# Kernel optimization log

Hardware: AMD Instinct MI355X
Metric: run time of the kernel (lower is better)

The kernel has to match this reference:

```python
import jax, jax.numpy as jnp
import numpy as np

B, N, D, H, K, R = 128, 2048, 256, 16, 32, 16
LEAKY_SLOPE = 0.01


def setup_inputs() -> dict:
    key = jax.random.key(0)
    ks = jax.random.split(key, 8)
    s = 0.05
    inp = jax.random.normal(ks[0], (B * N, D), dtype=jnp.float32)
    batch_ids = jnp.repeat(jnp.arange(B, dtype=jnp.int32), N)  # equal-size graphs
    Wk = jax.random.normal(ks[1], (K, D), dtype=jnp.float32) * s
    Wq0 = jax.random.normal(ks[2], (H * K, D), dtype=jnp.float32) * s
    Wq1 = jax.random.normal(ks[3], (H * K, D), dtype=jnp.float32) * s
    We = jax.random.normal(ks[4], (R, D), dtype=jnp.float32) * s
    Wout = jax.random.normal(ks[5], (D, H * R), dtype=jnp.float32) * s
    bout = jax.random.normal(ks[6], (D,), dtype=jnp.float32) * s
    return {"inp": inp, "batch_ids": batch_ids, "Wk": Wk, "Wq0": Wq0,
            "Wq1": Wq1, "We": We, "Wout": Wout, "bout": bout}


def reference(inp, batch_ids, Wk, Wq0, Wq1, We, Wout, bout):
    b = int(jnp.max(batch_ids)) + 1  # number of graphs (static at trace time)
    d = inp.shape[-1]
    # global max pool per graph (torch_geometric global_max_pool)
    pooled = jax.ops.segment_max(inp, batch_ids, num_segments=b)  # [B, D]
    x = inp.reshape(b, -1, d)                                     # [B, N, D]
    keys = jnp.einsum('bnd,kd->bnk', x, Wk)                       # [B, N, K]

    def head_embed(Wq):
        q = (pooled @ Wq.T).reshape(b, H, K)                      # [B, H, K]
        logits = jnp.einsum('bhk,bnk->bhn', q, keys)              # [B, H, N]
        att = jax.nn.softmax(logits, axis=-1)
        feat = jnp.einsum('bhn,bnd->bhd', att, x)                 # [B, H, D]
        return jnp.einsum('bhd,rd->bhr', feat, We)                # [B, H, R]

    dx = (head_embed(Wq0) - head_embed(Wq1)).reshape(b, -1)       # [B, H*R]
    out = dx @ Wout.T + bout
    return jnp.where(out >= 0, out, LEAKY_SLOPE * out)            # LeakyReLU
```

## Files before the change

### kernel.cpp

```cpp
#include <hip/hip_runtime.h>
#include <math.h>

#define B_ 128
#define N_ 2048
#define D_ 256
#define NHEADS 32
#define CHUNK 128
#define NCH 16

#define POOLEDP_OFF 0
#define PHI_OFF     524288
#define PLO_OFF     1048576
#define ML_OFF      1572864
#define FEATP_OFF   1703936

#define XHI_S  0
#define XLO_S  65536
#define ATT_S  131072
#define SMAX_S 139776
#define SSUM_S 140800
#define LDS_BYTES 141824

typedef __attribute__((ext_vector_type(8))) short short8;
typedef __attribute__((ext_vector_type(4))) float f32x4;

__device__ __forceinline__ unsigned short f2bf(float f) {
    unsigned u = __float_as_uint(f);
    u += 0x7fff + ((u >> 16) & 1);
    return (unsigned short)(u >> 16);
}
__device__ __forceinline__ float bf2f(unsigned short h) {
    return __uint_as_float(((unsigned)h) << 16);
}
__device__ __forceinline__ unsigned pack2bf(float a, float b) {
    return (unsigned)f2bf(a) | ((unsigned)f2bf(b) << 16);
}
__device__ __forceinline__ unsigned xsw(int row) {
    return (unsigned)((row ^ (row >> 3)) & 7) << 4;
}

__global__ __launch_bounds__(256) void k_pool(const float* __restrict__ inp,
                                              float* __restrict__ pooledp) {
    int b = blockIdx.x >> 4;
    int ch = blockIdx.x & 15;
    int t = threadIdx.x;
    int sub = t >> 6;
    int dq = (t & 63) * 4;
    const float* p = inp + ((size_t)(b * N_ + ch * 128 + sub)) * D_ + dq;
    float4 m = {-INFINITY, -INFINITY, -INFINITY, -INFINITY};
#pragma unroll 4
    for (int i = 0; i < 32; ++i) {
        float4 v = *(const float4*)(p + (size_t)i * 4 * D_);
        m.x = fmaxf(m.x, v.x); m.y = fmaxf(m.y, v.y);
        m.z = fmaxf(m.z, v.z); m.w = fmaxf(m.w, v.w);
    }
    __shared__ float sm[4 * 256];
    sm[sub * 256 + dq + 0] = m.x;
    sm[sub * 256 + dq + 1] = m.y;
    sm[sub * 256 + dq + 2] = m.z;
    sm[sub * 256 + dq + 3] = m.w;
    __syncthreads();
    float v = fmaxf(fmaxf(sm[t], sm[256 + t]), fmaxf(sm[512 + t], sm[768 + t]));
    pooledp[((size_t)ch * B_ + b) * 256 + t] = v;
}

__global__ __launch_bounds__(256) void k_qp(const float* __restrict__ pooledp,
                                            const float* __restrict__ Wq0,
                                            const float* __restrict__ Wq1,
                                            const float* __restrict__ Wk,
                                            unsigned short* __restrict__ Phi,
                                            unsigned short* __restrict__ Plo) {
    __shared__ float pl[D_];
    __shared__ float ql[1024];
    int b = blockIdx.x, t = threadIdx.x;
    float pv = -INFINITY;
#pragma unroll
    for (int i = 0; i < 16; ++i)
        pv = fmaxf(pv, pooledp[((size_t)i * B_ + b) * 256 + t]);
    pl[t] = pv;
    __syncthreads();
    for (int rep = 0; rep < 4; ++rep) {
        int idx = rep * 256 + t;
        const float* Wq = (idx < 512) ? Wq0 : Wq1;
        int row = idx & 511;
        const float4* wr = (const float4*)(Wq + (size_t)row * D_);
        float acc = 0.0f;
        for (int dqi = 0; dqi < 64; ++dqi) {
            float4 w = wr[dqi];
            const float* pp = &pl[dqi * 4];
            acc += w.x * pp[0] + w.y * pp[1] + w.z * pp[2] + w.w * pp[3];
        }
        ql[idx] = acc;
    }
    __syncthreads();
    float wk[32];
#pragma unroll
    for (int k = 0; k < 32; ++k) wk[k] = Wk[k * D_ + t];
    for (int j = 0; j < NHEADS; ++j) {
        const float* q = &ql[(j >> 4) * 512 + (j & 15) * 32];
        float acc = 0.0f;
#pragma unroll
        for (int k = 0; k < 32; ++k) acc = fmaf(q[k], wk[k], acc);
        unsigned short hi = f2bf(acc);
        unsigned short lo = f2bf(acc - bf2f(hi));
        Phi[((size_t)b * NHEADS + j) * D_ + t] = hi;
        Plo[((size_t)b * NHEADS + j) * D_ + t] = lo;
    }
}

__global__ __launch_bounds__(512, 2) void k_attn(const float* __restrict__ inp,
                                                 const unsigned short* __restrict__ Phi,
                                                 const unsigned short* __restrict__ Plo,
                                                 float* __restrict__ ml,
                                                 float* __restrict__ featp) {
    extern __shared__ unsigned char smem[];
    float* smax = (float*)(smem + SMAX_S);
    float* ssum = (float*)(smem + SSUM_S);

    int b = blockIdx.x >> 4, ns = blockIdx.x & 15;
    int t = threadIdx.x;
    int w = t >> 6;
    int lane = t & 63;
    int lq = lane >> 4;
    int lm = lane & 15;
    size_t gnode0 = (size_t)b * N_ + (size_t)ns * CHUNK;

#pragma unroll
    for (int i = 0; i < 16; ++i) {
        int row = i * 8 + w;
        float4 v = *(const float4*)(inp + (gnode0 + row) * D_ + lane * 4);
        ushort4 h4, l4;
        h4.x = f2bf(v.x); l4.x = f2bf(v.x - bf2f(h4.x));
        h4.y = f2bf(v.y); l4.y = f2bf(v.y - bf2f(h4.y));
        h4.z = f2bf(v.z); l4.z = f2bf(v.z - bf2f(h4.z));
        h4.w = f2bf(v.w); l4.w = f2bf(v.w - bf2f(h4.w));
        unsigned byteoff = (unsigned)row * 512u + (((unsigned)lane * 8u) ^ xsw(row));
        *(ushort4*)(smem + XHI_S + byteoff) = h4;
        *(ushort4*)(smem + XLO_S + byteoff) = l4;
    }
    __syncthreads();

    f32x4 acc_s[2];
    acc_s[0] = (f32x4){0.f, 0.f, 0.f, 0.f};
    acc_s[1] = (f32x4){0.f, 0.f, 0.f, 0.f};
    int arow = w * 16 + lm;
    unsigned abase = (unsigned)arow * 512u;
    unsigned asl = xsw(arow);
#pragma unroll
    for (int dc = 0; dc < 8; ++dc) {
        short8 bh[2], bl[2];
#pragma unroll
        for (int ht = 0; ht < 2; ++ht) {
            size_t poff = ((size_t)b * NHEADS + ht * 16 + lm) * D_ + dc * 32 + lq * 8;
            bh[ht] = *(const short8*)(Phi + poff);
            bl[ht] = *(const short8*)(Plo + poff);
        }
        unsigned doff = (((unsigned)(dc * 32 + lq * 8)) * 2u) ^ asl;
        short8 ah = *(const short8*)(smem + XHI_S + abase + doff);
        short8 al = *(const short8*)(smem + XLO_S + abase + doff);
#pragma unroll
        for (int ht = 0; ht < 2; ++ht) {
            acc_s[ht] = __builtin_amdgcn_mfma_f32_16x16x32_bf16(ah, bh[ht], acc_s[ht], 0, 0, 0);
            acc_s[ht] = __builtin_amdgcn_mfma_f32_16x16x32_bf16(ah, bl[ht], acc_s[ht], 0, 0, 0);
            acc_s[ht] = __builtin_amdgcn_mfma_f32_16x16x32_bf16(al, bh[ht], acc_s[ht], 0, 0, 0);
        }
    }

    float bm[2];
#pragma unroll
    for (int ht = 0; ht < 2; ++ht) {
        float m = fmaxf(fmaxf(acc_s[ht][0], acc_s[ht][1]),
                        fmaxf(acc_s[ht][2], acc_s[ht][3]));
        m = fmaxf(m, __shfl_xor(m, 16));
        m = fmaxf(m, __shfl_xor(m, 32));
        if (lane < 16) smax[w * 32 + ht * 16 + lane] = m;
    }
    __syncthreads();
#pragma unroll
    for (int ht = 0; ht < 2; ++ht) {
        float mm = smax[ht * 16 + lm];
#pragma unroll
        for (int w2 = 1; w2 < 8; ++w2) mm = fmaxf(mm, smax[w2 * 32 + ht * 16 + lm]);
        bm[ht] = mm;
    }
#pragma unroll
    for (int ht = 0; ht < 2; ++ht) {
        float e0 = __expf(acc_s[ht][0] - bm[ht]);
        float e1 = __expf(acc_s[ht][1] - bm[ht]);
        float e2 = __expf(acc_s[ht][2] - bm[ht]);
        float e3 = __expf(acc_s[ht][3] - bm[ht]);
        float s = (e0 + e1) + (e2 + e3);
        uint2 pk;
        pk.x = pack2bf(e0, e1);
        pk.y = pack2bf(e2, e3);
        *(uint2*)(smem + ATT_S + (size_t)(ht * 16 + lm) * 272 + w * 32 + lq * 8) = pk;
        s += __shfl_xor(s, 16);
        s += __shfl_xor(s, 32);
        if (lane < 16) ssum[w * 32 + ht * 16 + lane] = s;
    }
    __syncthreads();
    if (t < 32) {
        float mB = smax[t];
        float l = ssum[t];
#pragma unroll
        for (int w2 = 1; w2 < 8; ++w2) {
            mB = fmaxf(mB, smax[w2 * 32 + t]);
            l += ssum[w2 * 32 + t];
        }
        float* mlp = ml + ((size_t)(b * NHEADS + t) * NCH + ns) * 2;
        mlp[0] = mB;
        mlp[1] = l;
    }

    f32x4 acc_o[2][2];
#pragma unroll
    for (int ht = 0; ht < 2; ++ht)
#pragma unroll
        for (int dt = 0; dt < 2; ++dt) acc_o[ht][dt] = (f32x4){0.f, 0.f, 0.f, 0.f};

    int d0w = w * 32;
#pragma unroll
    for (int c = 0; c < 4; ++c) {
        short8 a0 = *(const short8*)(smem + ATT_S + (size_t)lm * 272 + c * 64 + lq * 16);
        short8 a1 = *(const short8*)(smem + ATT_S + (size_t)(16 + lm) * 272 + c * 64 + lq * 16);
#pragma unroll
        for (int dt = 0; dt < 2; ++dt) {
            unsigned d2 = (unsigned)(d0w + dt * 16 + lm) * 2u;
            int n0 = c * 32 + lq * 8;
            short8 bf;
#pragma unroll
            for (int j = 0; j < 8; ++j) {
                int n = n0 + j;
                unsigned byteoff = (unsigned)n * 512u + (d2 ^ xsw(n));
                bf[j] = *(const short*)(smem + XHI_S + byteoff);
            }
            acc_o[0][dt] = __builtin_amdgcn_mfma_f32_16x16x32_bf16(a0, bf, acc_o[0][dt], 0, 0, 0);
            acc_o[1][dt] = __builtin_amdgcn_mfma_f32_16x16x32_bf16(a1, bf, acc_o[1][dt], 0, 0, 0);
        }
    }
    float* fb = featp + ((size_t)(ns * B_ + b)) * D_ * NHEADS;
#pragma unroll
    for (int ht = 0; ht < 2; ++ht)
#pragma unroll
        for (int dt = 0; dt < 2; ++dt) {
            int d = d0w + dt * 16 + lm;
            int h0 = ht * 16 + lq * 4;
            *(f32x4*)(fb + (size_t)d * NHEADS + h0) = acc_o[ht][dt];
        }
}

__global__ __launch_bounds__(256) void k_out(const float* __restrict__ featp,
                                             const float* __restrict__ ml,
                                             const float* __restrict__ We,
                                             const float* __restrict__ Wout,
                                             const float* __restrict__ bout,
                                             float* __restrict__ out) {
    __shared__ float f[NHEADS * 257];
    __shared__ float bhrs[512];
    __shared__ float dxs[256];
    __shared__ float wns[NCH * 32];
    __shared__ float linv2[32];
    int b = blockIdx.x, t = threadIdx.x;
    if (t < 32) {
        const float* mlb = ml + ((size_t)b * NHEADS + t) * (NCH * 2);
        float M = mlb[0];
#pragma unroll
        for (int i = 1; i < NCH; ++i) M = fmaxf(M, mlb[2 * i]);
        float L = 0.0f;
#pragma unroll
        for (int i = 0; i < NCH; ++i) {
            float e = __expf(mlb[2 * i] - M);
            wns[i * 32 + t] = e;
            L += e * mlb[2 * i + 1];
        }
        linv2[t] = 1.0f / L;
    }
    __syncthreads();
    float fj[32];
#pragma unroll
    for (int j = 0; j < 32; ++j) fj[j] = 0.0f;
    for (int ns = 0; ns < NCH; ++ns) {
        const float* fp = featp + ((size_t)(ns * B_ + b) * D_ + t) * NHEADS;
#pragma unroll
        for (int j4 = 0; j4 < 8; ++j4) {
            float4 v = *(const float4*)(fp + j4 * 4);
            fj[j4 * 4 + 0] += wns[ns * 32 + j4 * 4 + 0] * v.x;
            fj[j4 * 4 + 1] += wns[ns * 32 + j4 * 4 + 1] * v.y;
            fj[j4 * 4 + 2] += wns[ns * 32 + j4 * 4 + 2] * v.z;
            fj[j4 * 4 + 3] += wns[ns * 32 + j4 * 4 + 3] * v.w;
        }
    }
#pragma unroll
    for (int j = 0; j < 32; ++j) f[j * 257 + t] = fj[j] * linv2[j];
    __syncthreads();
    for (int rep = 0; rep < 2; ++rep) {
        int idx = rep * 256 + t;
        int j = idx >> 4, r = idx & 15;
        const float* wrow = We + (size_t)r * D_;
        const float* ff = &f[j * 257];
        float acc = 0.0f;
        for (int d = 0; d < D_; ++d) acc = fmaf(ff[d], wrow[d], acc);
        bhrs[idx] = acc;
    }
    __syncthreads();
    {
        int h = t >> 4, r = t & 15;
        dxs[t] = bhrs[h * 16 + r] - bhrs[(16 + h) * 16 + r];
    }
    __syncthreads();
    float acc = bout[t];
    const float* wrow = Wout + (size_t)t * 256;
    for (int c = 0; c < 256; ++c) acc = fmaf(dxs[c], wrow[c], acc);
    out[(size_t)b * D_ + t] = acc >= 0.0f ? acc : 0.01f * acc;
}

extern "C" void kernel_launch(void* const* d_in, const int* in_sizes, int n_in,
                              void* d_out, int out_size, void* d_ws, size_t ws_size,
                              hipStream_t stream) {
    const float* inp  = (const float*)d_in[0];
    const float* Wk   = (const float*)d_in[2];
    const float* Wq0  = (const float*)d_in[3];
    const float* Wq1  = (const float*)d_in[4];
    const float* We   = (const float*)d_in[5];
    const float* Wout = (const float*)d_in[6];
    const float* bout = (const float*)d_in[7];
    float* out = (float*)d_out;
    float* ws  = (float*)d_ws;
    float* pooledp = ws + POOLEDP_OFF;
    unsigned short* Phi = (unsigned short*)(ws + PHI_OFF);
    unsigned short* Plo = (unsigned short*)(ws + PLO_OFF);
    float* ml     = ws + ML_OFF;
    float* featp  = ws + FEATP_OFF;

    static int lds_set = 0;
    if (!lds_set) {
        (void)hipFuncSetAttribute((const void*)k_attn,
                                  hipFuncAttributeMaxDynamicSharedMemorySize,
                                  LDS_BYTES);
        lds_set = 1;
    }

    k_pool<<<dim3(2048), dim3(256), 0, stream>>>(inp, pooledp);
    k_qp<<<dim3(128), dim3(256), 0, stream>>>(pooledp, Wq0, Wq1, Wk, Phi, Plo);
    k_attn<<<dim3(2048), dim3(512), LDS_BYTES, stream>>>(inp, Phi, Plo, ml, featp);
    k_out<<<dim3(128), dim3(256), 0, stream>>>(featp, ml, We, Wout, bout, out);
}
```

Baseline: 613.5 us.

## Loop over multiple node chunks per attention block with online softmax

Each attention block now iterates over four node chunks, keeping running max and sum in shared memory and rescaling the output accumulators (flash-style online softmax). This shrinks the grid and reduces the number of per-chunk partial feature and max/sum records written to global memory and re-read by the output kernel. In exchange the chunks are processed serially with extra barriers per chunk, and fewer blocks are available to hide memory latency.

Result: faster. 598.4 us (-2.5%).

```diff
diff --git a/kernel.cpp b/kernel.cpp
--- a/kernel.cpp
+++ b/kernel.cpp
@@ -6,20 +6,24 @@
 #define D_ 256
 #define NHEADS 32
 #define CHUNK 128
-#define NCH 16
+#define CPB 4
+#define NBLK 4
 
 #define POOLEDP_OFF 0
 #define PHI_OFF     524288
 #define PLO_OFF     1048576
 #define ML_OFF      1572864
-#define FEATP_OFF   1703936
+#define FEATP_OFF   1605632
 
 #define XHI_S  0
 #define XLO_S  65536
 #define ATT_S  131072
 #define SMAX_S 139776
 #define SSUM_S 140800
-#define LDS_BYTES 141824
+#define MRUN_S 141824
+#define LRUN_S 141952
+#define RESC_S 142080
+#define LDS_BYTES 142208
 
 typedef __attribute__((ext_vector_type(8))) short short8;
 typedef __attribute__((ext_vector_type(4))) float f32x4;
@@ -116,129 +120,154 @@
     extern __shared__ unsigned char smem[];
     float* smax = (float*)(smem + SMAX_S);
     float* ssum = (float*)(smem + SSUM_S);
-
-    int b = blockIdx.x >> 4, ns = blockIdx.x & 15;
+    float* mrun = (float*)(smem + MRUN_S);
+    float* lrun = (float*)(smem + LRUN_S);
+    float* resc = (float*)(smem + RESC_S);
+
+    int b = blockIdx.x >> 2, blk = blockIdx.x & 3;
     int t = threadIdx.x;
     int w = t >> 6;
     int lane = t & 63;
     int lq = lane >> 4;
     int lm = lane & 15;
-    size_t gnode0 = (size_t)b * N_ + (size_t)ns * CHUNK;
-
-#pragma unroll
-    for (int i = 0; i < 16; ++i) {
-        int row = i * 8 + w;
-        float4 v = *(const float4*)(inp + (gnode0 + row) * D_ + lane * 4);
-        ushort4 h4, l4;
-        h4.x = f2bf(v.x); l4.x = f2bf(v.x - bf2f(h4.x));
-        h4.y = f2bf(v.y); l4.y = f2bf(v.y - bf2f(h4.y));
-        h4.z = f2bf(v.z); l4.z = f2bf(v.z - bf2f(h4.z));
-        h4.w = f2bf(v.w); l4.w = f2bf(v.w - bf2f(h4.w));
-        unsigned byteoff = (unsigned)row * 512u + (((unsigned)lane * 8u) ^ xsw(row));
-        *(ushort4*)(smem + XHI_S + byteoff) = h4;
-        *(ushort4*)(smem + XLO_S + byteoff) = l4;
-    }
-    __syncthreads();
-
-    f32x4 acc_s[2];
-    acc_s[0] = (f32x4){0.f, 0.f, 0.f, 0.f};
-    acc_s[1] = (f32x4){0.f, 0.f, 0.f, 0.f};
+
+    if (t < 32) { mrun[t] = -INFINITY; lrun[t] = 0.0f; }
+
+    f32x4 acc_o[2][2];
+#pragma unroll
+    for (int ht = 0; ht < 2; ++ht)
+#pragma unroll
+        for (int dt = 0; dt < 2; ++dt) acc_o[ht][dt] = (f32x4){0.f, 0.f, 0.f, 0.f};
+
     int arow = w * 16 + lm;
     unsigned abase = (unsigned)arow * 512u;
     unsigned asl = xsw(arow);
-#pragma unroll
-    for (int dc = 0; dc < 8; ++dc) {
-        short8 bh[2], bl[2];
+    int d0w = w * 32;
+
+#pragma unroll 1
+    for (int ch = 0; ch < CPB; ++ch) {
+        size_t gnode0 = (size_t)b * N_ + (size_t)(blk * CPB + ch) * CHUNK;
+
+        __syncthreads();
+#pragma unroll
+        for (int i = 0; i < 16; ++i) {
+            int row = i * 8 + w;
+            float4 v = *(const float4*)(inp + (gnode0 + row) * D_ + lane * 4);
+            ushort4 h4, l4;
+            h4.x = f2bf(v.x); l4.x = f2bf(v.x - bf2f(h4.x));
+            h4.y = f2bf(v.y); l4.y = f2bf(v.y - bf2f(h4.y));
+            h4.z = f2bf(v.z); l4.z = f2bf(v.z - bf2f(h4.z));
+            h4.w = f2bf(v.w); l4.w = f2bf(v.w - bf2f(h4.w));
+            unsigned byteoff = (unsigned)row * 512u + (((unsigned)lane * 8u) ^ xsw(row));
+            *(ushort4*)(smem + XHI_S + byteoff) = h4;
+            *(ushort4*)(smem + XLO_S + byteoff) = l4;
+        }
+        __syncthreads();
+
+        f32x4 acc_s[2];
+        acc_s[0] = (f32x4){0.f, 0.f, 0.f, 0.f};
+        acc_s[1] = (f32x4){0.f, 0.f, 0.f, 0.f};
+#pragma unroll
+        for (int dc = 0; dc < 8; ++dc) {
+            short8 bh[2], bl[2];
+#pragma unroll
+            for (int ht = 0; ht < 2; ++ht) {
+                size_t poff = ((size_t)b * NHEADS + ht * 16 + lm) * D_ + dc * 32 + lq * 8;
+                bh[ht] = *(const short8*)(Phi + poff);
+                bl[ht] = *(const short8*)(Plo + poff);
+            }
+            unsigned doff = (((unsigned)(dc * 32 + lq * 8)) * 2u) ^ asl;
+            short8 ah = *(const short8*)(smem + XHI_S + abase + doff);
+            short8 al = *(const short8*)(smem + XLO_S + abase + doff);
+#pragma unroll
+            for (int ht = 0; ht < 2; ++ht) {
+                acc_s[ht] = __builtin_amdgcn_mfma_f32_16x16x32_bf16(ah, bh[ht], acc_s[ht], 0, 0, 0);
+                acc_s[ht] = __builtin_amdgcn_mfma_f32_16x16x32_bf16(ah, bl[ht], acc_s[ht], 0, 0, 0);
+                acc_s[ht] = __builtin_amdgcn_mfma_f32_16x16x32_bf16(al, bh[ht], acc_s[ht], 0, 0, 0);
+            }
+        }
+
 #pragma unroll
         for (int ht = 0; ht < 2; ++ht) {
-            size_t poff = ((size_t)b * NHEADS + ht * 16 + lm) * D_ + dc * 32 + lq * 8;
-            bh[ht] = *(const short8*)(Phi + poff);
-            bl[ht] = *(const short8*)(Plo + poff);
-        }
-        unsigned doff = (((unsigned)(dc * 32 + lq * 8)) * 2u) ^ asl;
-        short8 ah = *(const short8*)(smem + XHI_S + abase + doff);
-        short8 al = *(const short8*)(smem + XLO_S + abase + doff);
+            float m = fmaxf(fmaxf(acc_s[ht][0], acc_s[ht][1]),
+                            fmaxf(acc_s[ht][2], acc_s[ht][3]));
+            m = fmaxf(m, __shfl_xor(m, 16));
+            m = fmaxf(m, __shfl_xor(m, 32));
+            if (lane < 16) smax[w * 32 + ht * 16 + lane] = m;
+        }
+        __syncthreads();
+        if (t < 32) {
+            float mc = smax[t];
+#pragma unroll
+            for (int w2 = 1; w2 < 8; ++w2) mc = fmaxf(mc, smax[w2 * 32 + t]);
+            float mold = mrun[t];
+            float mnew = fmaxf(mold, mc);
+            resc[t] = __expf(mold - mnew);
+            mrun[t] = mnew;
+        }
+        __syncthreads();
 #pragma unroll
         for (int ht = 0; ht < 2; ++ht) {
-            acc_s[ht] = __builtin_amdgcn_mfma_f32_16x16x32_bf16(ah, bh[ht], acc_s[ht], 0, 0, 0);
-            acc_s[ht] = __builtin_amdgcn_mfma_f32_16x16x32_bf16(ah, bl[ht], acc_s[ht], 0, 0, 0);
-            acc_s[ht] = __builtin_amdgcn_mfma_f32_16x16x32_bf16(al, bh[ht], acc_s[ht], 0, 0, 0);
-        }
-    }
-
-    float bm[2];
-#pragma unroll
-    for (int ht = 0; ht < 2; ++ht) {
-        float m = fmaxf(fmaxf(acc_s[ht][0], acc_s[ht][1]),
-                        fmaxf(acc_s[ht][2], acc_s[ht][3]));
-        m = fmaxf(m, __shfl_xor(m, 16));
-        m = fmaxf(m, __shfl_xor(m, 32));
-        if (lane < 16) smax[w * 32 + ht * 16 + lane] = m;
-    }
-    __syncthreads();
-#pragma unroll
-    for (int ht = 0; ht < 2; ++ht) {
-        float mm = smax[ht * 16 + lm];
-#pragma unroll
-        for (int w2 = 1; w2 < 8; ++w2) mm = fmaxf(mm, smax[w2 * 32 + ht * 16 + lm]);
-        bm[ht] = mm;
-    }
-#pragma unroll
-    for (int ht = 0; ht < 2; ++ht) {
-        float e0 = __expf(acc_s[ht][0] - bm[ht]);
-        float e1 = __expf(acc_s[ht][1] - bm[ht]);
-        float e2 = __expf(acc_s[ht][2] - bm[ht]);
-        float e3 = __expf(acc_s[ht][3] - bm[ht]);
-        float s = (e0 + e1) + (e2 + e3);
-        uint2 pk;
-        pk.x = pack2bf(e0, e1);
-        pk.y = pack2bf(e2, e3);
-        *(uint2*)(smem + ATT_S + (size_t)(ht * 16 + lm) * 272 + w * 32 + lq * 8) = pk;
-        s += __shfl_xor(s, 16);
-        s += __shfl_xor(s, 32);
-        if (lane < 16) ssum[w * 32 + ht * 16 + lane] = s;
-    }
-    __syncthreads();
+            f32x4 rs = *(const f32x4*)(resc + ht * 16 + lq * 4);
+#pragma unroll
+            for (int dt = 0; dt < 2; ++dt) {
+#pragma unroll
+                for (int r = 0; r < 4; ++r) acc_o[ht][dt][r] *= rs[r];
+            }
+        }
+        float bm[2];
+        bm[0] = mrun[lm];
+        bm[1] = mrun[16 + lm];
+#pragma unroll
+        for (int ht = 0; ht < 2; ++ht) {
+            float e0 = __expf(acc_s[ht][0] - bm[ht]);
+            float e1 = __expf(acc_s[ht][1] - bm[ht]);
+            float e2 = __expf(acc_s[ht][2] - bm[ht]);
+            float e3 = __expf(acc_s[ht][3] - bm[ht]);
+            float s = (e0 + e1) + (e2 + e3);
+            uint2 pk;
+            pk.x = pack2bf(e0, e1);
+            pk.y = pack2bf(e2, e3);
+            *(uint2*)(smem + ATT_S + (size_t)(ht * 16 + lm) * 272 + w * 32 + lq * 8) = pk;
+            s += __shfl_xor(s, 16);
+            s += __shfl_xor(s, 32);
+            if (lane < 16) ssum[w * 32 + ht * 16 + lane] = s;
+        }
+        __syncthreads();
+        if (t < 32) {
+            float l = ssum[t];
+#pragma unroll
+            for (int w2 = 1; w2 < 8; ++w2) l += ssum[w2 * 32 + t];
+            lrun[t] = lrun[t] * resc[t] + l;
+        }
+
+#pragma unroll
+        for (int c = 0; c < 4; ++c) {
+            short8 a0 = *(const short8*)(smem + ATT_S + (size_t)lm * 272 + c * 64 + lq * 16);
+            short8 a1 = *(const short8*)(smem + ATT_S + (size_t)(16 + lm) * 272 + c * 64 + lq * 16);
+#pragma unroll
+            for (int dt = 0; dt < 2; ++dt) {
+                unsigned d2 = (unsigned)(d0w + dt * 16 + lm) * 2u;
+                int n0 = c * 32 + lq * 8;
+                short8 bf;
+#pragma unroll
+                for (int j = 0; j < 8; ++j) {
+                    int n = n0 + j;
+                    unsigned byteoff = (unsigned)n * 512u + (d2 ^ xsw(n));
+                    bf[j] = *(const short*)(smem + XHI_S + byteoff);
+                }
+                acc_o[0][dt] = __builtin_amdgcn_mfma_f32_16x16x32_bf16(a0, bf, acc_o[0][dt], 0, 0, 0);
+                acc_o[1][dt] = __builtin_amdgcn_mfma_f32_16x16x32_bf16(a1, bf, acc_o[1][dt], 0, 0, 0);
+            }
+        }
+    }
+
     if (t < 32) {
-        float mB = smax[t];
-        float l = ssum[t];
-#pragma unroll
-        for (int w2 = 1; w2 < 8; ++w2) {
-            mB = fmaxf(mB, smax[w2 * 32 + t]);
-            l += ssum[w2 * 32 + t];
-        }
-        float* mlp = ml + ((size_t)(b * NHEADS + t) * NCH + ns) * 2;
-        mlp[0] = mB;
-        mlp[1] = l;
-    }
-
-    f32x4 acc_o[2][2];
-#pragma unroll
-    for (int ht = 0; ht < 2; ++ht)
-#pragma unroll
-        for (int dt = 0; dt < 2; ++dt) acc_o[ht][dt] = (f32x4){0.f, 0.f, 0.f, 0.f};
-
-    int d0w = w * 32;
-#pragma unroll
-    for (int c = 0; c < 4; ++c) {
-        short8 a0 = *(const short8*)(smem + ATT_S + (size_t)lm * 272 + c * 64 + lq * 16);
-        short8 a1 = *(const short8*)(smem + ATT_S + (size_t)(16 + lm) * 272 + c * 64 + lq * 16);
-#pragma unroll
-        for (int dt = 0; dt < 2; ++dt) {
-            unsigned d2 = (unsigned)(d0w + dt * 16 + lm) * 2u;
-            int n0 = c * 32 + lq * 8;
-            short8 bf;
-#pragma unroll
-            for (int j = 0; j < 8; ++j) {
-                int n = n0 + j;
-                unsigned byteoff = (unsigned)n * 512u + (d2 ^ xsw(n));
-                bf[j] = *(const short*)(smem + XHI_S + byteoff);
-            }
-            acc_o[0][dt] = __builtin_amdgcn_mfma_f32_16x16x32_bf16(a0, bf, acc_o[0][dt], 0, 0, 0);
-            acc_o[1][dt] = __builtin_amdgcn_mfma_f32_16x16x32_bf16(a1, bf, acc_o[1][dt], 0, 0, 0);
-        }
-    }
-    float* fb = featp + ((size_t)(ns * B_ + b)) * D_ * NHEADS;
+        float* mlp = ml + ((size_t)(b * NHEADS + t) * NBLK + blk) * 2;
+        mlp[0] = mrun[t];
+        mlp[1] = lrun[t];
+    }
+    float* fb = featp + ((size_t)(blk * B_ + b)) * D_ * NHEADS;
 #pragma unroll
     for (int ht = 0; ht < 2; ++ht)
 #pragma unroll
@@ -258,28 +287,25 @@
     __shared__ float f[NHEADS * 257];
     __shared__ float bhrs[512];
     __shared__ float dxs[256];
-    __shared__ float wns[NCH * 32];
+    __shared__ float wns[NBLK * 32];
     __shared__ float linv2[32];
     int b = blockIdx.x, t = threadIdx.x;
     if (t < 32) {
-        const float* mlb = ml + ((size_t)b * NHEADS + t) * (NCH * 2);
-        float M = mlb[0];
-#pragma unroll
-        for (int i = 1; i < NCH; ++i) M = fmaxf(M, mlb[2 * i]);
-        float L = 0.0f;
-#pragma unroll
-        for (int i = 0; i < NCH; ++i) {
-            float e = __expf(mlb[2 * i] - M);
-            wns[i * 32 + t] = e;
-            L += e * mlb[2 * i + 1];
-        }
+        const float* mlb = ml + ((size_t)b * NHEADS + t) * (NBLK * 2);
+        float M = fmaxf(fmaxf(mlb[0], mlb[2]), fmaxf(mlb[4], mlb[6]));
+        float e0 = __expf(mlb[0] - M), e1 = __expf(mlb[2] - M);
+        float e2 = __expf(mlb[4] - M), e3 = __expf(mlb[6] - M);
+        float L = e0 * mlb[1] + e1 * mlb[3] + e2 * mlb[5] + e3 * mlb[7];
+        wns[0 * 32 + t] = e0; wns[1 * 32 + t] = e1;
+        wns[2 * 32 + t] = e2; wns[3 * 32 + t] = e3;
         linv2[t] = 1.0f / L;
     }
     __syncthreads();
     float fj[32];
 #pragma unroll
     for (int j = 0; j < 32; ++j) fj[j] = 0.0f;
-    for (int ns = 0; ns < NCH; ++ns) {
+#pragma unroll 1
+    for (int ns = 0; ns < NBLK; ++ns) {
         const float* fp = featp + ((size_t)(ns * B_ + b) * D_ + t) * NHEADS;
 #pragma unroll
         for (int j4 = 0; j4 < 8; ++j4) {
@@ -342,6 +368,6 @@
 
     k_pool<<<dim3(2048), dim3(256), 0, stream>>>(inp, pooledp);
     k_qp<<<dim3(128), dim3(256), 0, stream>>>(pooledp, Wq0, Wq1, Wk, Phi, Plo);
-    k_attn<<<dim3(2048), dim3(512), LDS_BYTES, stream>>>(inp, Phi, Plo, ml, featp);
+    k_attn<<<dim3(512), dim3(512), LDS_BYTES, stream>>>(inp, Phi, Plo, ml, featp);
     k_out<<<dim3(128), dim3(256), 0, stream>>>(featp, ml, We, Wout, bout, out);
 }
```
